# Optimization experiments

Hardware: AMD Instinct MI355X
Metric: run time of the kernel (lower is better)

## Reference

```python
import jax, jax.numpy as jnp
import numpy as np

B, S, D, H, DH = 4, 2048, 1024, 16, 64

def setup_inputs() -> dict:
    key = jax.random.key(0)
    ks = jax.random.split(key, 8)
    scale = 1.0 / np.sqrt(D)  # mimic lecun_normal-ish scaling
    return {
        "inputs_q": jax.random.normal(ks[0], (B, S, D), jnp.float32),
        "inputs_kv": jax.random.normal(ks[1], (B, S, D), jnp.float32),
        "Wq": jax.random.normal(ks[2], (D, H, DH), jnp.float32) * scale,
        "bq": jnp.zeros((H, DH), jnp.float32),
        "Wk": jax.random.normal(ks[3], (D, H, DH), jnp.float32) * scale,
        "bk": jnp.zeros((H, DH), jnp.float32),
        "Wv": jax.random.normal(ks[4], (D, H, DH), jnp.float32) * scale,
        "bv": jnp.zeros((H, DH), jnp.float32),
        "Wo": jax.random.normal(ks[5], (H, DH, D), jnp.float32) * (1.0 / np.sqrt(H * DH)),
        "bo": jnp.zeros((D,), jnp.float32),
    }

def reference(inputs_q, inputs_kv, Wq, bq, Wk, bk, Wv, bv, Wo, bo):
    # QKV projections: [B,S,D] x [D,H,Dh] -> [B,S,H,Dh]
    q = jnp.einsum('bsd,dhf->bshf', inputs_q, Wq) + bq
    k = jnp.einsum('bsd,dhf->bshf', inputs_kv, Wk) + bk
    v = jnp.einsum('bsd,dhf->bshf', inputs_kv, Wv) + bv
    q = q / jnp.sqrt(jnp.asarray(DH, q.dtype))
    # attention scores [B,H,Sq,Sk]
    scores = jnp.einsum('bqhf,bkhf->bhqk', q, k)
    probs = jax.nn.softmax(scores, axis=-1)
    x = jnp.einsum('bhqk,bkhf->bqhf', probs, v)
    # output projection over (H, Dh)
    out = jnp.einsum('bqhf,hfd->bqd', x, Wo) + bo
    return out
```

## Files before the change

kernel.cpp:

```cpp
#include <hip/hip_runtime.h>
#include <hip/hip_bf16.h>
#include <hip/hip_fp16.h>
#include <math.h>

#define B_   4
#define S_   2048
#define D_   1024
#define H_   16
#define DH_  64
#define M_   (B_ * S_)
#define N_   (H_ * DH_)

typedef _Float16 f16;
typedef __attribute__((ext_vector_type(2))) _Float16 f16x2;
typedef __attribute__((ext_vector_type(4))) _Float16 f16x4;
typedef __attribute__((ext_vector_type(8))) _Float16 f16x8;
typedef __attribute__((ext_vector_type(4))) float    f32x4;

union H8 { f16x8 v; f16x4 q[2]; f16x2 d[4]; };
union PK { __half2 h2; f16x2 v; };

#if __has_builtin(__builtin_amdgcn_exp2f)
__device__ __forceinline__ float exp2_fast(float x) { return __builtin_amdgcn_exp2f(x); }
#else
__device__ __forceinline__ float exp2_fast(float x) {
  float r; asm("v_exp_f32 %0, %1" : "=v"(r) : "v"(x)); return r;
}
#endif

__device__ __forceinline__ void async_cp16(const void* g, void* l) {
  __builtin_amdgcn_global_load_lds(
      (const __attribute__((address_space(1))) unsigned int*)g,
      (__attribute__((address_space(3))) unsigned int*)l, 16, 0, 0);
}

__global__ __launch_bounds__(256) void cvt_f32_f16(const float* __restrict__ in,
                                                   f16* __restrict__ out, int n4) {
  int i = blockIdx.x * 256 + threadIdx.x;
  if (i < n4) {
    f32x4 v = ((const f32x4*)in)[i];
    ((f16x4*)out)[i] = __builtin_convertvector(v, f16x4);
  }
}

__global__ __launch_bounds__(256) void transpose_w(
    const float* __restrict__ W0, const float* __restrict__ W1,
    const float* __restrict__ W2, const float* __restrict__ W3,
    f16* __restrict__ T0, f16* __restrict__ T1,
    f16* __restrict__ T2, f16* __restrict__ T3) {
  const float* W = (blockIdx.z == 0) ? W0 : (blockIdx.z == 1) ? W1
                 : (blockIdx.z == 2) ? W2 : W3;
  f16* T = (blockIdx.z == 0) ? T0 : (blockIdx.z == 1) ? T1
         : (blockIdx.z == 2) ? T2 : T3;
  __shared__ float tile[32][33];
  int x  = blockIdx.x * 32 + threadIdx.x;
  int y0 = blockIdx.y * 32 + threadIdx.y;
#pragma unroll
  for (int i = 0; i < 32; i += 8)
    tile[threadIdx.y + i][threadIdx.x] = W[(size_t)(y0 + i) * 1024 + x];
  __syncthreads();
  int tx  = blockIdx.y * 32 + threadIdx.x;
  int ty0 = blockIdx.x * 32 + threadIdx.y;
#pragma unroll
  for (int i = 0; i < 32; i += 8)
    T[(size_t)(ty0 + i) * 1024 + tx] = (f16)tile[threadIdx.x][threadIdx.y + i];
}

__global__ __launch_bounds__(256) void transpose_v(const f16* __restrict__ v,
                                                   f16* __restrict__ vt) {
  int bh = blockIdx.y;
  int b  = bh >> 4, h = bh & 15;
  int s0 = blockIdx.x * 64;
  __shared__ f16 tile[64][72];
  int tid = threadIdx.x;
#pragma unroll
  for (int it = 0; it < 16; ++it) {
    int idx = it * 256 + tid;
    int r = idx >> 6, c = idx & 63;
    tile[r][c] = v[((size_t)(b * S_ + s0 + r)) * N_ + h * DH_ + c];
  }
  __syncthreads();
#pragma unroll
  for (int it = 0; it < 16; ++it) {
    int idx = it * 256 + tid;
    int fr = idx >> 6, sc = idx & 63;
    vt[((size_t)bh * DH_ + fr) * S_ + s0 + sc] = tile[sc][fr];
  }
}

__global__ __launch_bounds__(256) void gemm_qkv(
    const f16* __restrict__ Aq, const f16* __restrict__ Akv,
    const f16* __restrict__ WqT, const f16* __restrict__ WkT, const f16* __restrict__ WvT,
    const float* __restrict__ bq, const float* __restrict__ bk, const float* __restrict__ bv,
    float qscale, f16* __restrict__ oq, f16* __restrict__ ok, f16* __restrict__ ov) {
  __shared__ f16 lA[2][128 * 64];
  __shared__ f16 lB[2][128 * 64];
  const int cpx = gridDim.x >> 3;
  const int wg  = (blockIdx.x & 7) * cpx + (blockIdx.x >> 3);
  const int tile_m = (wg / 24) * 128;
  const int nt = wg % 24, part = nt >> 3;
  const int tile_n = (nt & 7) * 128;
  const f16* A  = (part == 0) ? Aq : Akv;
  const f16* Bt = ((part == 0) ? WqT : (part == 1) ? WkT : WvT) + (size_t)tile_n * D_;
  const float* bias = ((part == 0) ? bq : (part == 1) ? bk : bv) + tile_n;
  f16* outp = ((part == 0) ? oq : (part == 1) ? ok : ov);
  const float scale = (part == 0) ? qscale : 1.0f;

  const int tid  = threadIdx.x;
  const int lane = tid & 63, wid = tid >> 6;
  const int wr = wid >> 1, wc = wid & 1;
  const int l8 = lane >> 3, c8 = (lane & 7) * 8;
  const int r15 = lane & 15, hi = lane >> 4;

  f32x4 acc[4][4];
#pragma unroll
  for (int m = 0; m < 4; ++m)
#pragma unroll
    for (int n = 0; n < 4; ++n) acc[m][n] = (f32x4)(0.f);

  auto STAGE = [&](int t, int buf) {
    int kt = t * 64;
#pragma unroll
    for (int i = 0; i < 4; ++i) {
      int rb = wid * 32 + i * 8;
      async_cp16(A  + (size_t)(tile_m + rb + l8) * D_ + kt + c8, &lA[buf][rb * 64]);
      async_cp16(Bt + (size_t)(rb + l8) * D_ + kt + c8, &lB[buf][rb * 64]);
    }
  };

  STAGE(0, 0);
  __syncthreads();
  for (int t = 0; t < D_ / 64; ++t) {
    const int cur = t & 1;
    if (t + 1 < D_ / 64) STAGE(t + 1, cur ^ 1);
#pragma unroll
    for (int kk = 0; kk < 2; ++kk) {
      f16x8 af[4], bf[4];
#pragma unroll
      for (int m = 0; m < 4; ++m)
        af[m] = *(const f16x8*)&lA[cur][(wr * 64 + m * 16 + r15) * 64 + kk * 32 + hi * 8];
#pragma unroll
      for (int n = 0; n < 4; ++n)
        bf[n] = *(const f16x8*)&lB[cur][(wc * 64 + n * 16 + r15) * 64 + kk * 32 + hi * 8];
#pragma unroll
      for (int m = 0; m < 4; ++m)
#pragma unroll
        for (int n = 0; n < 4; ++n)
          acc[m][n] = __builtin_amdgcn_mfma_f32_16x16x32_f16(af[m], bf[n], acc[m][n], 0, 0, 0);
    }
    __syncthreads();
  }

#pragma unroll
  for (int m = 0; m < 4; ++m) {
    int row0 = tile_m + wr * 64 + m * 16 + hi * 4;
#pragma unroll
    for (int n = 0; n < 4; ++n) {
      int col = wc * 64 + n * 16 + r15;
      float bv_ = bias[col];
#pragma unroll
      for (int r = 0; r < 4; ++r) {
        float v = (acc[m][n][r] + bv_) * scale;
        outp[(size_t)(row0 + r) * N_ + tile_n + col] = (f16)v;
      }
    }
  }
}

__global__ __launch_bounds__(256) void gemm_out(
    const f16* __restrict__ A, const f16* __restrict__ Bt,
    const float* __restrict__ bias, float* __restrict__ outp,
    int M, int N, int K) {
  __shared__ f16 lA[2][128 * 64];
  __shared__ f16 lB[2][128 * 64];
  const int nbx = N >> 7;
  const int cpx = gridDim.x >> 3;
  const int wg  = (blockIdx.x & 7) * cpx + (blockIdx.x >> 3);
  const int tile_m = (wg / nbx) * 128, tile_n = (wg % nbx) * 128;
  const int tid  = threadIdx.x;
  const int lane = tid & 63, wid = tid >> 6;
  const int wr = wid >> 1, wc = wid & 1;
  const int l8 = lane >> 3, c8 = (lane & 7) * 8;
  const int r15 = lane & 15, hi = lane >> 4;

  f32x4 acc[4][4];
#pragma unroll
  for (int m = 0; m < 4; ++m)
#pragma unroll
    for (int n = 0; n < 4; ++n) acc[m][n] = (f32x4)(0.f);

  auto STAGE = [&](int t, int buf) {
    int kt = t * 64;
#pragma unroll
    for (int i = 0; i < 4; ++i) {
      int rb = wid * 32 + i * 8;
      async_cp16(A  + (size_t)(tile_m + rb + l8) * K + kt + c8, &lA[buf][rb * 64]);
      async_cp16(Bt + (size_t)(tile_n + rb + l8) * K + kt + c8, &lB[buf][rb * 64]);
    }
  };

  STAGE(0, 0);
  __syncthreads();
  const int T = K / 64;
  for (int t = 0; t < T; ++t) {
    const int cur = t & 1;
    if (t + 1 < T) STAGE(t + 1, cur ^ 1);
#pragma unroll
    for (int kk = 0; kk < 2; ++kk) {
      f16x8 af[4], bf[4];
#pragma unroll
      for (int m = 0; m < 4; ++m)
        af[m] = *(const f16x8*)&lA[cur][(wr * 64 + m * 16 + r15) * 64 + kk * 32 + hi * 8];
#pragma unroll
      for (int n = 0; n < 4; ++n)
        bf[n] = *(const f16x8*)&lB[cur][(wc * 64 + n * 16 + r15) * 64 + kk * 32 + hi * 8];
#pragma unroll
      for (int m = 0; m < 4; ++m)
#pragma unroll
        for (int n = 0; n < 4; ++n)
          acc[m][n] = __builtin_amdgcn_mfma_f32_16x16x32_f16(af[m], bf[n], acc[m][n], 0, 0, 0);
    }
    __syncthreads();
  }

#pragma unroll
  for (int m = 0; m < 4; ++m) {
    int row0 = tile_m + wr * 64 + m * 16 + hi * 4;
#pragma unroll
    for (int n = 0; n < 4; ++n) {
      int col = tile_n + wc * 64 + n * 16 + r15;
      float bv = bias[col];
#pragma unroll
      for (int r = 0; r < 4; ++r)
        outp[(size_t)(row0 + r) * N + col] = acc[m][n][r] + bv;
    }
  }
}

__global__ __launch_bounds__(256, 2) void attn(
    const f16* __restrict__ q, const f16* __restrict__ k,
    const f16* __restrict__ vt, f16* __restrict__ x) {
  __shared__ f16 lK[2][64 * 64];
  __shared__ f16 lV[2][64 * 64];
  const int tid = threadIdx.x, lane = tid & 63, wid = tid >> 6;
  const int bh = blockIdx.y, b = bh >> 4, h = bh & 15;
  const int q0 = blockIdx.x * 256 + wid * 64;
  const int c15 = lane & 15, hi = lane >> 4;
  const int swr = (c15 & 7) << 4;
  const int swz = 8 * ((lane & 7) ^ (lane >> 3));
  const int lrow = lane >> 3;

  const f16* qb = q  + (size_t)b * S_ * N_ + h * DH_;
  const f16* kb = k  + (size_t)b * S_ * N_ + h * DH_;
  const f16* vb = vt + (size_t)bh * DH_ * S_;

  f16x8 qf[4][2];
#pragma unroll
  for (int qm = 0; qm < 4; ++qm)
#pragma unroll
    for (int kk = 0; kk < 2; ++kk)
      qf[qm][kk] = *(const f16x8*)(qb + (size_t)(q0 + qm * 16 + c15) * N_ + kk * 32 + hi * 8);

  f32x4 xa[4][4];
#pragma unroll
  for (int fn = 0; fn < 4; ++fn)
#pragma unroll
    for (int qm = 0; qm < 4; ++qm) xa[fn][qm] = (f32x4)(0.f);
  float rm[4], rl[4];
#pragma unroll
  for (int qm = 0; qm < 4; ++qm) { rm[qm] = -INFINITY; rl[qm] = 0.f; }

  auto STAGE = [&](int t, int buf) {
    int j0 = t * 64;
#pragma unroll
    for (int i = 0; i < 2; ++i) {
      int rb = wid * 16 + i * 8;
      async_cp16(kb + (size_t)(j0 + rb + lrow) * N_ + swz, &lK[buf][rb * 64]);
      async_cp16(vb + (size_t)(rb + lrow) * S_ + j0 + swz, &lV[buf][rb * 64]);
    }
  };

  STAGE(0, 0);
  __syncthreads();

  for (int t = 0; t < S_ / 64; ++t) {
    const int cur = t & 1;
    if (t < S_ / 64 - 1) STAGE(t + 1, cur ^ 1);

    f16x8 kf[4][2];
#pragma unroll
    for (int jn = 0; jn < 4; ++jn) {
      int rowe = (jn * 16 + c15) * 64;
#pragma unroll
      for (int kk = 0; kk < 2; ++kk)
        kf[jn][kk] = *(const f16x8*)&lK[cur][rowe + (((kk * 64 + hi * 16) ^ swr) >> 1)];
    }

    f16x8 bfrag[4][2];
#pragma unroll
    for (int qm = 0; qm < 4; ++qm) {
      f32x4 sq[4];
#pragma unroll
      for (int jn = 0; jn < 4; ++jn) sq[jn] = (f32x4)(0.f);
      __builtin_amdgcn_s_setprio(1);
#pragma unroll
      for (int kk = 0; kk < 2; ++kk)
#pragma unroll
        for (int jn = 0; jn < 4; ++jn)
          sq[jn] = __builtin_amdgcn_mfma_f32_16x16x32_f16(kf[jn][kk], qf[qm][kk], sq[jn], 0, 0, 0);
      __builtin_amdgcn_s_setprio(0);

      float mx = sq[0][0];
#pragma unroll
      for (int jn = 0; jn < 4; ++jn)
#pragma unroll
        for (int r = 0; r < 4; ++r) mx = fmaxf(mx, sq[jn][r]);
      mx = fmaxf(mx, __shfl_xor(mx, 16));
      mx = fmaxf(mx, __shfl_xor(mx, 32));

      float p[4][4], ts = 0.f;
      if (__all(mx - rm[qm] <= 8.0f)) {
#pragma unroll
        for (int jn = 0; jn < 4; ++jn)
#pragma unroll
          for (int r = 0; r < 4; ++r) {
            p[jn][r] = exp2_fast(sq[jn][r] - rm[qm]);
            ts += p[jn][r];
          }
        ts += __shfl_xor(ts, 16);
        ts += __shfl_xor(ts, 32);
        rl[qm] += ts;
      } else {
        float nm  = fmaxf(rm[qm], mx);
        float fac = exp2_fast(rm[qm] - nm);
        rm[qm] = nm;
#pragma unroll
        for (int jn = 0; jn < 4; ++jn)
#pragma unroll
          for (int r = 0; r < 4; ++r) {
            p[jn][r] = exp2_fast(sq[jn][r] - nm);
            ts += p[jn][r];
          }
        ts += __shfl_xor(ts, 16);
        ts += __shfl_xor(ts, 32);
        rl[qm] = rl[qm] * fac + ts;
#pragma unroll
        for (int fn = 0; fn < 4; ++fn)
#pragma unroll
          for (int r = 0; r < 4; ++r) xa[fn][qm][r] *= fac;
      }

      PK w[4][2];
#pragma unroll
      for (int jn = 0; jn < 4; ++jn)
#pragma unroll
        for (int hh = 0; hh < 2; ++hh)
          w[jn][hh].h2 = __floats2half2_rn(p[jn][2 * hh], p[jn][2 * hh + 1]);
#pragma unroll
      for (int kk = 0; kk < 2; ++kk) {
        H8 u;
        u.d[0] = w[2 * kk][0].v;     u.d[1] = w[2 * kk][1].v;
        u.d[2] = w[2 * kk + 1][0].v; u.d[3] = w[2 * kk + 1][1].v;
        bfrag[qm][kk] = u.v;
      }
    }

    __builtin_amdgcn_s_setprio(1);
#pragma unroll
    for (int kk = 0; kk < 2; ++kk)
#pragma unroll
      for (int fn = 0; fn < 4; ++fn) {
        int rowe = (fn * 16 + c15) * 64;
        H8 u;
        u.q[0] = *(const f16x4*)&lV[cur][rowe + (((kk * 64 + hi * 8) ^ swr) >> 1)];
        u.q[1] = *(const f16x4*)&lV[cur][rowe + (((kk * 64 + 32 + hi * 8) ^ swr) >> 1)];
#pragma unroll
        for (int qm = 0; qm < 4; ++qm)
          xa[fn][qm] = __builtin_amdgcn_mfma_f32_16x16x32_f16(u.v, bfrag[qm][kk], xa[fn][qm], 0, 0, 0);
      }
    __builtin_amdgcn_s_setprio(0);
    __syncthreads();
  }

  float inv[4];
#pragma unroll
  for (int qm = 0; qm < 4; ++qm) inv[qm] = 1.f / rl[qm];
#pragma unroll
  for (int qm = 0; qm < 4; ++qm) {
    size_t rowb = (size_t)(b * S_ + q0 + qm * 16 + c15) * N_ + h * DH_;
#pragma unroll
    for (int fn = 0; fn < 4; ++fn) {
      f16x4 o;
#pragma unroll
      for (int r = 0; r < 4; ++r) o[r] = (f16)(xa[fn][qm][r] * inv[qm]);
      *(f16x4*)(x + rowb + fn * 16 + hi * 4) = o;
    }
  }
}

extern "C" void kernel_launch(void* const* d_in, const int* in_sizes, int n_in,
                              void* d_out, int out_size, void* d_ws, size_t ws_size,
                              hipStream_t stream) {
  const float* inq  = (const float*)d_in[0];
  const float* inkv = (const float*)d_in[1];
  const float* Wq = (const float*)d_in[2];
  const float* bq = (const float*)d_in[3];
  const float* Wk = (const float*)d_in[4];
  const float* bk = (const float*)d_in[5];
  const float* Wv = (const float*)d_in[6];
  const float* bv = (const float*)d_in[7];
  const float* Wo = (const float*)d_in[8];
  const float* bo = (const float*)d_in[9];
  float* out = (float*)d_out;

  char* ws = (char*)d_ws;
  const size_t MB = 1024 * 1024;
  f16* h_inq  = (f16*)(ws + 0);
  f16* h_inkv = (f16*)(ws + 16 * MB);
  f16* h_WqT  = (f16*)(ws + 32 * MB);
  f16* h_WkT  = (f16*)(ws + 34 * MB);
  f16* h_WvT  = (f16*)(ws + 36 * MB);
  f16* h_WoT  = (f16*)(ws + 38 * MB);
  f16* h_q    = (f16*)(ws + 40 * MB);
  f16* h_k    = (f16*)(ws + 56 * MB);
  f16* h_v    = (f16*)(ws + 72 * MB);
  f16* h_vt   = h_inq;
  f16* h_x    = h_inkv;

  const int nIn = M_ * D_;
  cvt_f32_f16<<<nIn / 4 / 256, 256, 0, stream>>>(inq,  h_inq,  nIn / 4);
  cvt_f32_f16<<<nIn / 4 / 256, 256, 0, stream>>>(inkv, h_inkv, nIn / 4);
  transpose_w<<<dim3(32, 32, 4), dim3(32, 8), 0, stream>>>(
      Wq, Wk, Wv, Wo, h_WqT, h_WkT, h_WvT, h_WoT);
  const float qscale = 0.125f * 1.4426950408889634f;
  gemm_qkv<<<1536, 256, 0, stream>>>(h_inq, h_inkv, h_WqT, h_WkT, h_WvT,
                                     bq, bk, bv, qscale, h_q, h_k, h_v);
  transpose_v<<<dim3(S_ / 64, B_ * H_), 256, 0, stream>>>(h_v, h_vt);
  attn<<<dim3(S_ / 256, B_ * H_), 256, 0, stream>>>(h_q, h_k, h_vt, h_x);
  gemm_out<<<(M_ / 128) * (N_ / 128), 256, 0, stream>>>(h_x, h_WoT, bo, out, M_, N_, D_);
}
```

Measured before the change: 373.0 us.

## Rework projection GEMMs to 8-wave 128x256 tiles with triple-buffered swizzled LDS

```diff
diff --git a/kernel.cpp b/kernel.cpp
--- a/kernel.cpp
+++ b/kernel.cpp
@@ -88,29 +88,34 @@
   }
 }
 
-__global__ __launch_bounds__(256) void gemm_qkv(
+
+__global__ __launch_bounds__(512, 4) void gemm_qkv8(
     const f16* __restrict__ Aq, const f16* __restrict__ Akv,
-    const f16* __restrict__ WqT, const f16* __restrict__ WkT, const f16* __restrict__ WvT,
+    const f16* __restrict__ WqkvT,
     const float* __restrict__ bq, const float* __restrict__ bk, const float* __restrict__ bv,
     float qscale, f16* __restrict__ oq, f16* __restrict__ ok, f16* __restrict__ ov) {
-  __shared__ f16 lA[2][128 * 64];
-  __shared__ f16 lB[2][128 * 64];
+  __shared__ f16 lA[3][128 * 32];
+  __shared__ f16 lB[3][256 * 32];
   const int cpx = gridDim.x >> 3;
   const int wg  = (blockIdx.x & 7) * cpx + (blockIdx.x >> 3);
-  const int tile_m = (wg / 24) * 128;
-  const int nt = wg % 24, part = nt >> 3;
-  const int tile_n = (nt & 7) * 128;
+  const int tile_m = (wg / 12) * 128;
+  const int nt = wg % 12, part = nt >> 2, tile_np = (nt & 3) * 256;
   const f16* A  = (part == 0) ? Aq : Akv;
-  const f16* Bt = ((part == 0) ? WqT : (part == 1) ? WkT : WvT) + (size_t)tile_n * D_;
-  const float* bias = ((part == 0) ? bq : (part == 1) ? bk : bv) + tile_n;
-  f16* outp = ((part == 0) ? oq : (part == 1) ? ok : ov);
+  const f16* Bt = WqkvT + ((size_t)part << 20) + (size_t)tile_np * 1024;
+  const float* bias = ((part == 0) ? bq : (part == 1) ? bk : bv) + tile_np;
+  f16* outp = (part == 0) ? oq : (part == 1) ? ok : ov;
   const float scale = (part == 0) ? qscale : 1.0f;
 
-  const int tid  = threadIdx.x;
-  const int lane = tid & 63, wid = tid >> 6;
-  const int wr = wid >> 1, wc = wid & 1;
-  const int l8 = lane >> 3, c8 = (lane & 7) * 8;
+  const int tid = threadIdx.x, lane = tid & 63, wid = tid >> 6;
+  const int wr = wid >> 2, wc = wid & 3;
   const int r15 = lane & 15, hi = lane >> 4;
+  const int srow = lane >> 2;
+  const int scol = 8 * ((lane & 3) ^ ((lane >> 3) & 3));
+  const int fslot = 8 * (hi ^ ((r15 >> 1) & 3));
+
+  const f16* sA  = A  + (size_t)(tile_m + wid * 16 + srow) * 1024 + scol;
+  const f16* sB0 = Bt + (size_t)(wid * 16 + srow) * 1024 + scol;
+  const f16* sB1 = sB0 + (size_t)128 * 1024;
 
   f32x4 acc[4][4];
 #pragma unroll
@@ -118,37 +123,43 @@
 #pragma unroll
     for (int n = 0; n < 4; ++n) acc[m][n] = (f32x4)(0.f);
 
-  auto STAGE = [&](int t, int buf) {
-    int kt = t * 64;
-#pragma unroll
-    for (int i = 0; i < 4; ++i) {
-      int rb = wid * 32 + i * 8;
-      async_cp16(A  + (size_t)(tile_m + rb + l8) * D_ + kt + c8, &lA[buf][rb * 64]);
-      async_cp16(Bt + (size_t)(rb + l8) * D_ + kt + c8, &lB[buf][rb * 64]);
-    }
+  auto STAGE = [&](int t, int sl) {
+    async_cp16(sA  + t * 32, &lA[sl][wid * 512]);
+    async_cp16(sB0 + t * 32, &lB[sl][wid * 512]);
+    async_cp16(sB1 + t * 32, &lB[sl][4096 + wid * 512]);
   };
 
   STAGE(0, 0);
-  __syncthreads();
-  for (int t = 0; t < D_ / 64; ++t) {
-    const int cur = t & 1;
-    if (t + 1 < D_ / 64) STAGE(t + 1, cur ^ 1);
-#pragma unroll
-    for (int kk = 0; kk < 2; ++kk) {
-      f16x8 af[4], bf[4];
-#pragma unroll
-      for (int m = 0; m < 4; ++m)
-        af[m] = *(const f16x8*)&lA[cur][(wr * 64 + m * 16 + r15) * 64 + kk * 32 + hi * 8];
+  STAGE(1, 1);
+  asm volatile("s_waitcnt vmcnt(3)" ::: "memory");
+  __builtin_amdgcn_s_barrier();
+
+  int s = 0;
+  for (int c = 0; c < 32; ++c) {
+    f16x8 af[4], bf[4];
+#pragma unroll
+    for (int m = 0; m < 4; ++m)
+      af[m] = *(const f16x8*)&lA[s][(wr * 64 + m * 16 + r15) * 32 + fslot];
+#pragma unroll
+    for (int n = 0; n < 4; ++n)
+      bf[n] = *(const f16x8*)&lB[s][(wc * 64 + n * 16 + r15) * 32 + fslot];
+    if (c + 2 < 32) {
+      int s2 = s + 2; if (s2 >= 3) s2 -= 3;
+      STAGE(c + 2, s2);
+      asm volatile("s_waitcnt vmcnt(3)" ::: "memory");
+    } else {
+      asm volatile("s_waitcnt vmcnt(0)" ::: "memory");
+    }
+    __builtin_amdgcn_s_barrier();
+    __builtin_amdgcn_s_setprio(1);
+#pragma unroll
+    for (int m = 0; m < 4; ++m)
 #pragma unroll
       for (int n = 0; n < 4; ++n)
-        bf[n] = *(const f16x8*)&lB[cur][(wc * 64 + n * 16 + r15) * 64 + kk * 32 + hi * 8];
-#pragma unroll
-      for (int m = 0; m < 4; ++m)
-#pragma unroll
-        for (int n = 0; n < 4; ++n)
-          acc[m][n] = __builtin_amdgcn_mfma_f32_16x16x32_f16(af[m], bf[n], acc[m][n], 0, 0, 0);
-    }
-    __syncthreads();
+        acc[m][n] = __builtin_amdgcn_mfma_f32_16x16x32_f16(af[m], bf[n], acc[m][n], 0, 0, 0);
+    __builtin_amdgcn_s_setprio(0);
+    __builtin_amdgcn_s_barrier();
+    ++s; if (s == 3) s = 0;
   }
 
 #pragma unroll
@@ -161,27 +172,32 @@
 #pragma unroll
       for (int r = 0; r < 4; ++r) {
         float v = (acc[m][n][r] + bv_) * scale;
-        outp[(size_t)(row0 + r) * N_ + tile_n + col] = (f16)v;
+        outp[(size_t)(row0 + r) * N_ + tile_np + col] = (f16)v;
       }
     }
   }
 }
 
-__global__ __launch_bounds__(256) void gemm_out(
+__global__ __launch_bounds__(512, 4) void gemm_out8(
     const f16* __restrict__ A, const f16* __restrict__ Bt,
-    const float* __restrict__ bias, float* __restrict__ outp,
-    int M, int N, int K) {
-  __shared__ f16 lA[2][128 * 64];
-  __shared__ f16 lB[2][128 * 64];
-  const int nbx = N >> 7;
+    const float* __restrict__ bias, float* __restrict__ outp) {
+  __shared__ f16 lA[3][128 * 32];
+  __shared__ f16 lB[3][256 * 32];
   const int cpx = gridDim.x >> 3;
   const int wg  = (blockIdx.x & 7) * cpx + (blockIdx.x >> 3);
-  const int tile_m = (wg / nbx) * 128, tile_n = (wg % nbx) * 128;
-  const int tid  = threadIdx.x;
-  const int lane = tid & 63, wid = tid >> 6;
-  const int wr = wid >> 1, wc = wid & 1;
-  const int l8 = lane >> 3, c8 = (lane & 7) * 8;
+  const int tile_m = (wg >> 2) * 128;
+  const int tile_n = (wg & 3) * 256;
+
+  const int tid = threadIdx.x, lane = tid & 63, wid = tid >> 6;
+  const int wr = wid >> 2, wc = wid & 3;
   const int r15 = lane & 15, hi = lane >> 4;
+  const int srow = lane >> 2;
+  const int scol = 8 * ((lane & 3) ^ ((lane >> 3) & 3));
+  const int fslot = 8 * (hi ^ ((r15 >> 1) & 3));
+
+  const f16* sA  = A  + (size_t)(tile_m + wid * 16 + srow) * 1024 + scol;
+  const f16* sB0 = Bt + (size_t)(tile_n + wid * 16 + srow) * 1024 + scol;
+  const f16* sB1 = sB0 + (size_t)128 * 1024;
 
   f32x4 acc[4][4];
 #pragma unroll
@@ -189,38 +205,43 @@
 #pragma unroll
     for (int n = 0; n < 4; ++n) acc[m][n] = (f32x4)(0.f);
 
-  auto STAGE = [&](int t, int buf) {
-    int kt = t * 64;
-#pragma unroll
-    for (int i = 0; i < 4; ++i) {
-      int rb = wid * 32 + i * 8;
-      async_cp16(A  + (size_t)(tile_m + rb + l8) * K + kt + c8, &lA[buf][rb * 64]);
-      async_cp16(Bt + (size_t)(tile_n + rb + l8) * K + kt + c8, &lB[buf][rb * 64]);
-    }
+  auto STAGE = [&](int t, int sl) {
+    async_cp16(sA  + t * 32, &lA[sl][wid * 512]);
+    async_cp16(sB0 + t * 32, &lB[sl][wid * 512]);
+    async_cp16(sB1 + t * 32, &lB[sl][4096 + wid * 512]);
   };
 
   STAGE(0, 0);
-  __syncthreads();
-  const int T = K / 64;
-  for (int t = 0; t < T; ++t) {
-    const int cur = t & 1;
-    if (t + 1 < T) STAGE(t + 1, cur ^ 1);
-#pragma unroll
-    for (int kk = 0; kk < 2; ++kk) {
-      f16x8 af[4], bf[4];
-#pragma unroll
-      for (int m = 0; m < 4; ++m)
-        af[m] = *(const f16x8*)&lA[cur][(wr * 64 + m * 16 + r15) * 64 + kk * 32 + hi * 8];
+  STAGE(1, 1);
+  asm volatile("s_waitcnt vmcnt(3)" ::: "memory");
+  __builtin_amdgcn_s_barrier();
+
+  int s = 0;
+  for (int c = 0; c < 32; ++c) {
+    f16x8 af[4], bf[4];
+#pragma unroll
+    for (int m = 0; m < 4; ++m)
+      af[m] = *(const f16x8*)&lA[s][(wr * 64 + m * 16 + r15) * 32 + fslot];
+#pragma unroll
+    for (int n = 0; n < 4; ++n)
+      bf[n] = *(const f16x8*)&lB[s][(wc * 64 + n * 16 + r15) * 32 + fslot];
+    if (c + 2 < 32) {
+      int s2 = s + 2; if (s2 >= 3) s2 -= 3;
+      STAGE(c + 2, s2);
+      asm volatile("s_waitcnt vmcnt(3)" ::: "memory");
+    } else {
+      asm volatile("s_waitcnt vmcnt(0)" ::: "memory");
+    }
+    __builtin_amdgcn_s_barrier();
+    __builtin_amdgcn_s_setprio(1);
+#pragma unroll
+    for (int m = 0; m < 4; ++m)
 #pragma unroll
       for (int n = 0; n < 4; ++n)
-        bf[n] = *(const f16x8*)&lB[cur][(wc * 64 + n * 16 + r15) * 64 + kk * 32 + hi * 8];
-#pragma unroll
-      for (int m = 0; m < 4; ++m)
-#pragma unroll
-        for (int n = 0; n < 4; ++n)
-          acc[m][n] = __builtin_amdgcn_mfma_f32_16x16x32_f16(af[m], bf[n], acc[m][n], 0, 0, 0);
-    }
-    __syncthreads();
+        acc[m][n] = __builtin_amdgcn_mfma_f32_16x16x32_f16(af[m], bf[n], acc[m][n], 0, 0, 0);
+    __builtin_amdgcn_s_setprio(0);
+    __builtin_amdgcn_s_barrier();
+    ++s; if (s == 3) s = 0;
   }
 
 #pragma unroll
@@ -232,7 +253,7 @@
       float bv = bias[col];
 #pragma unroll
       for (int r = 0; r < 4; ++r)
-        outp[(size_t)(row0 + r) * N + col] = acc[m][n][r] + bv;
+        outp[(size_t)(row0 + r) * N_ + col] = acc[m][n][r] + bv;
     }
   }
 }
@@ -433,9 +454,9 @@
   transpose_w<<<dim3(32, 32, 4), dim3(32, 8), 0, stream>>>(
       Wq, Wk, Wv, Wo, h_WqT, h_WkT, h_WvT, h_WoT);
   const float qscale = 0.125f * 1.4426950408889634f;
-  gemm_qkv<<<1536, 256, 0, stream>>>(h_inq, h_inkv, h_WqT, h_WkT, h_WvT,
+  gemm_qkv8<<<768, 512, 0, stream>>>(h_inq, h_inkv, h_WqT,
                                      bq, bk, bv, qscale, h_q, h_k, h_v);
   transpose_v<<<dim3(S_ / 64, B_ * H_), 256, 0, stream>>>(h_v, h_vt);
   attn<<<dim3(S_ / 256, B_ * H_), 256, 0, stream>>>(h_q, h_k, h_vt, h_x);
-  gemm_out<<<(M_ / 128) * (N_ / 128), 256, 0, stream>>>(h_x, h_WoT, bo, out, M_, N_, D_);
-}
+  gemm_out8<<<256, 512, 0, stream>>>(h_x, h_WoT, bo, out);
+}
```

Result: faster. 340.6 us (-8.7%).
